# Optimization experiments

Measured on AMD Instinct MI355X. Metric: run time of the kernel, lower is better.

Reference implementation:

```python
import jax, jax.numpy as jnp
import numpy as np

GROUPS = 32
EPS = 1e-3  # keras GroupNormalization default epsilon

def group_norm(x, gamma, beta):
    B, H, W, C = x.shape
    g = GROUPS
    xg = x.reshape(B, H, W, g, C // g)
    mean = jnp.mean(xg, axis=(1, 2, 4), keepdims=True)
    var = jnp.var(xg, axis=(1, 2, 4), keepdims=True)
    xn = (xg - mean) * jax.lax.rsqrt(var + EPS)
    xn = xn.reshape(B, H, W, C)
    return xn * gamma + beta

def setup_inputs() -> dict:
    key = jax.random.key(0)
    ks = jax.random.split(key, 8)
    B, H, W, C = 16, 32, 32, 512
    s = C ** -0.5
    return {
        "x": jax.random.normal(ks[0], (B, H, W, C), jnp.float32),
        "gamma": jnp.ones((C,), jnp.float32),
        "beta": jnp.zeros((C,), jnp.float32),
        "wq": jax.random.normal(ks[1], (C, C), jnp.float32) * s,
        "bq": jnp.zeros((C,), jnp.float32),
        "wk": jax.random.normal(ks[2], (C, C), jnp.float32) * s,
        "bk": jnp.zeros((C,), jnp.float32),
        "wv": jax.random.normal(ks[3], (C, C), jnp.float32) * s,
        "bv": jnp.zeros((C,), jnp.float32),
        "wp": jax.random.normal(ks[4], (C, C), jnp.float32) * s,
        "bp": jnp.zeros((C,), jnp.float32),
        "index": 0,
    }

def reference(x, gamma, beta, wq, bq, wk, bk, wv, bv, wp, bp, index):
    B, H, W, C = x.shape
    N = H * W
    residual = x
    xn = group_norm(x, gamma, beta)
    xf = xn.reshape(B, N, C)
    q = xf @ wq + bq
    k = xf @ wk + bk
    v = xf @ wv + bv
    # full self-attention over all H*W positions (single head)
    scores = jnp.einsum('bnc,bmc->bnm', q, k) * (C ** -0.5)  # [B, N, N]
    attn = jax.nn.softmax(scores, axis=-1)
    out = jnp.einsum('bnm,bmc->bnc', attn, v)
    out = out @ wp + bp
    return out.reshape(B, H, W, C) + residual
```

## Files before the change

kernel.cpp:

```cpp
#include <hip/hip_runtime.h>

typedef __bf16 bf16;
typedef __bf16 bf16x8 __attribute__((ext_vector_type(8)));
typedef __bf16 bf16x4 __attribute__((ext_vector_type(4)));
typedef float  f32x4  __attribute__((ext_vector_type(4)));

#define CDIM   512
#define NPOS   1024
#define NBATCH 16
#define MTOT   (NBATCH * NPOS)
#define WELEMS (CDIM * CDIM)

#define OFF_WT  ((size_t)0)
#define OFF_XN  ((size_t)(2 * 1024 * 1024))
#define OFF_Q   (OFF_XN + (size_t)MTOT * CDIM * 2)
#define OFF_K   (OFF_Q  + (size_t)MTOT * CDIM * 2)
#define OFF_VT  (OFF_K  + (size_t)MTOT * CDIM * 2)
#define OFF_O   OFF_XN

__device__ __forceinline__ void gload16(const bf16* g, bf16* l) {
    __builtin_amdgcn_global_load_lds(
        (const __attribute__((address_space(1))) void*)g,
        (__attribute__((address_space(3))) void*)l, 16, 0, 0);
}

__device__ __forceinline__ unsigned int pk2(float lo, float hi) {
    union { bf16 h; unsigned short s; } a, c;
    a.h = (bf16)lo; c.h = (bf16)hi;
    return (unsigned int)a.s | ((unsigned int)c.s << 16);
}

__global__ __launch_bounds__(256) void transpose_cast(
    const float* __restrict__ w0, const float* __restrict__ w1,
    const float* __restrict__ w2, const float* __restrict__ w3,
    bf16* __restrict__ wt)
{
    __shared__ bf16 tile[32][33];
    int z = blockIdx.z;
    const float* W = (z == 0) ? w0 : (z == 1) ? w1 : (z == 2) ? w2 : w3;
    bf16* out = wt + (size_t)z * WELEMS;
    int bx = blockIdx.x * 32;
    int by = blockIdx.y * 32;
    int tx = threadIdx.x & 31, ty = threadIdx.x >> 5;
    #pragma unroll
    for (int i = ty; i < 32; i += 8)
        tile[i][tx] = (bf16)W[(size_t)(by + i) * CDIM + bx + tx];
    __syncthreads();
    #pragma unroll
    for (int i = ty; i < 32; i += 8)
        out[(size_t)(bx + i) * CDIM + by + tx] = tile[tx][i];
}

__global__ __launch_bounds__(256) void groupnorm_kernel(
    const float* __restrict__ x, const float* __restrict__ gamma,
    const float* __restrict__ beta, bf16* __restrict__ xn)
{
    int b = blockIdx.x >> 5;
    int g = blockIdx.x & 31;
    const float* xb = x + (size_t)b * NPOS * CDIM;
    int t = threadIdx.x, lane = t & 63, wid = t >> 6;

    float s = 0.f, s2 = 0.f;
    for (int i = t; i < 4096; i += 256) {
        int n = i >> 2, c4 = i & 3;
        const float4 v = *(const float4*)&xb[n * CDIM + g * 16 + c4 * 4];
        s  += v.x + v.y + v.z + v.w;
        s2 += v.x * v.x + v.y * v.y + v.z * v.z + v.w * v.w;
    }
    #pragma unroll
    for (int o = 32; o; o >>= 1) { s += __shfl_xor(s, o); s2 += __shfl_xor(s2, o); }
    __shared__ float rs[4], rs2[4];
    if (lane == 0) { rs[wid] = s; rs2[wid] = s2; }
    __syncthreads();
    float S  = rs[0] + rs[1] + rs[2] + rs[3];
    float S2 = rs2[0] + rs2[1] + rs2[2] + rs2[3];
    const float inv_n = 1.f / 16384.f;
    float mean = S * inv_n;
    float var  = S2 * inv_n - mean * mean;
    float rstd = rsqrtf(var + 1e-3f);

    bf16* xnb = xn + (size_t)b * NPOS * CDIM;
    for (int i = t; i < 4096; i += 256) {
        int n = i >> 2, c4 = i & 3;
        int c = g * 16 + c4 * 4;
        const float4 v = *(const float4*)&xb[n * CDIM + c];
        bf16x4 o;
        o[0] = (bf16)(((v.x - mean) * rstd) * gamma[c + 0] + beta[c + 0]);
        o[1] = (bf16)(((v.y - mean) * rstd) * gamma[c + 1] + beta[c + 1]);
        o[2] = (bf16)(((v.z - mean) * rstd) * gamma[c + 2] + beta[c + 2]);
        o[3] = (bf16)(((v.w - mean) * rstd) * gamma[c + 3] + beta[c + 3]);
        *(bf16x4*)&xnb[n * CDIM + c] = o;
    }
}

#define BM 128
#define BN 128
#define BK 32

__global__ __launch_bounds__(256) void gemm_qkv(
    const bf16* __restrict__ A, const bf16* __restrict__ Bw,
    const float* __restrict__ bq, const float* __restrict__ bk,
    const float* __restrict__ bv, float qscale,
    bf16* __restrict__ Qo, bf16* __restrict__ Ko, bf16* __restrict__ Vto)
{
    __shared__ __align__(16) bf16 lsa[BM * BK];
    __shared__ __align__(16) bf16 lsb[BN * BK];
    const int bm = blockIdx.x * BM;
    const int bnG = blockIdx.y * BN;
    const int region = blockIdx.y >> 2;
    const int t = threadIdx.x;
    const int lane = t & 63;
    const int wid = t >> 6;
    const int wr = (wid >> 1) * 64;
    const int wc = (wid & 1) * 64;
    const int lr = lane & 15;
    const int ks = lane >> 4;

    const int r0 = t >> 2, c0 = (t & 3) * 8;
    const int r1 = (t + 256) >> 2, c1 = ((t + 256) & 3) * 8;

    f32x4 acc[4][4] = {};

    for (int k0 = 0; k0 < CDIM; k0 += BK) {
        gload16(&A[(size_t)(bm + r0) * CDIM + k0 + c0], &lsa[t * 8]);
        gload16(&A[(size_t)(bm + r1) * CDIM + k0 + c1], &lsa[(t + 256) * 8]);
        gload16(&Bw[(size_t)(bnG + r0) * CDIM + k0 + c0], &lsb[t * 8]);
        gload16(&Bw[(size_t)(bnG + r1) * CDIM + k0 + c1], &lsb[(t + 256) * 8]);
        __syncthreads();
        bf16x8 af[4], bfr[4];
        #pragma unroll
        for (int m = 0; m < 4; m++)
            af[m] = *(const bf16x8*)&lsa[(wr + m * 16 + lr) * BK + ks * 8];
        #pragma unroll
        for (int n = 0; n < 4; n++)
            bfr[n] = *(const bf16x8*)&lsb[(wc + n * 16 + lr) * BK + ks * 8];
        #pragma unroll
        for (int m = 0; m < 4; m++)
            #pragma unroll
            for (int n = 0; n < 4; n++)
                acc[m][n] = __builtin_amdgcn_mfma_f32_16x16x32_bf16(af[m], bfr[n], acc[m][n], 0, 0, 0);
        __syncthreads();
    }

    const float* bias = (region == 0) ? bq : (region == 1) ? bk : bv;
    const float scale = (region == 0) ? qscale : 1.f;
    #pragma unroll
    for (int m = 0; m < 4; m++) {
        #pragma unroll
        for (int n = 0; n < 4; n++) {
            const int row0 = bm + wr + m * 16 + ks * 4;
            const int colG = bnG + wc + n * 16 + lr;
            const int cl = colG - region * CDIM;
            const float bvl = bias[cl];
            #pragma unroll
            for (int r = 0; r < 4; r++) {
                const int rr = row0 + r;
                const float v = (acc[m][n][r] + bvl) * scale;
                if (region == 0) {
                    Qo[(size_t)rr * CDIM + cl] = (bf16)v;
                } else if (region == 1) {
                    Ko[(size_t)rr * CDIM + cl] = (bf16)v;
                } else {
                    const int bb = rr >> 10, nn = rr & 1023;
                    Vto[(size_t)bb * CDIM * NPOS + (size_t)cl * NPOS + nn] = (bf16)v;
                }
            }
        }
    }
}

#define QT 64
#define KVB 64

__global__ __launch_bounds__(256, 1) void flash_attn(
    const bf16* __restrict__ Q, const bf16* __restrict__ K,
    const bf16* __restrict__ Vt, bf16* __restrict__ O)
{
    __shared__ __align__(16) bf16 Klds[KVB * CDIM];
    __shared__ __align__(16) bf16 Vlds[CDIM * KVB];
    __shared__ unsigned int Plds[4][16 * 35];

    const int p  = blockIdx.x;
    const int b  = (p & 7) + 8 * ((p >> 3) >> 4);
    const int qt = (p >> 3) & 15;

    const int t = threadIdx.x;
    const int lane = t & 63;
    const int w = t >> 6;
    const int lr = lane & 15;
    const int g  = lane >> 4;

    const bf16* Qg = Q  + ((size_t)b * NPOS + qt * QT) * CDIM;
    const bf16* Kg = K  + (size_t)b * NPOS * CDIM;
    const bf16* Vg = Vt + (size_t)b * CDIM * NPOS;

    bf16x8 qf[16];
    {
        const bf16* qrow = Qg + (size_t)(w * 16 + lr) * CDIM + g * 8;
        #pragma unroll
        for (int ds = 0; ds < 16; ds++)
            qf[ds] = *(const bf16x8*)(qrow + ds * 32);
    }

    f32x4 acc[32];
    #pragma unroll
    for (int i = 0; i < 32; i++) acc[i] = (f32x4){0.f, 0.f, 0.f, 0.f};
    float m_run = -1e30f, l_run = 0.f;
    unsigned int* Pw = Plds[w];

    #pragma unroll
    for (int i = 0; i < 16; i++) {
        int ci = t + i * 256;
        int r = ci >> 6, c = ci & 63;
        gload16(Kg + (size_t)r * CDIM + ((c ^ (r & 7)) * 8), &Klds[ci * 8]);
    }
    __syncthreads();

    for (int kt = 0; kt < 16; kt++) {
        {
            const int kv0 = kt * KVB;
            #pragma unroll
            for (int i = 0; i < 16; i++) {
                int ci = t + i * 256;
                int r = ci >> 3, c = ci & 7;
                gload16(Vg + (size_t)r * NPOS + kv0 + ((c ^ (r & 7)) * 8), &Vlds[ci * 8]);
            }
        }
        f32x4 s[4] = {};
        #pragma unroll
        for (int ds = 0; ds < 16; ds++) {
            #pragma unroll
            for (int k16 = 0; k16 < 4; k16++) {
                const int row = k16 * 16 + lr;
                const bf16x8 kf = *(const bf16x8*)&Klds[row * CDIM + (((ds * 4 + g) ^ (row & 7)) * 8)];
                s[k16] = __builtin_amdgcn_mfma_f32_16x16x32_bf16(kf, qf[ds], s[k16], 0, 0, 0);
            }
        }
        float mt = -1e30f;
        #pragma unroll
        for (int k16 = 0; k16 < 4; k16++)
            #pragma unroll
            for (int r = 0; r < 4; r++) mt = fmaxf(mt, s[k16][r]);
        mt = fmaxf(mt, __shfl_xor(mt, 16));
        mt = fmaxf(mt, __shfl_xor(mt, 32));
        const float m_new = (mt > m_run + 8.f) ? mt : m_run;
        float pr[16];
        float ts = 0.f;
        #pragma unroll
        for (int k16 = 0; k16 < 4; k16++)
            #pragma unroll
            for (int r = 0; r < 4; r++) {
                float e = __expf(s[k16][r] - m_new);
                pr[k16 * 4 + r] = e; ts += e;
            }
        ts += __shfl_xor(ts, 16);
        ts += __shfl_xor(ts, 32);
        if (__any(m_new != m_run)) {
            const float alpha = __expf(m_run - m_new);
            #pragma unroll
            for (int i = 0; i < 32; i++) {
                acc[i][0] *= alpha; acc[i][1] *= alpha;
                acc[i][2] *= alpha; acc[i][3] *= alpha;
            }
            l_run *= alpha;
        }
        l_run += ts;
        m_run = m_new;
        #pragma unroll
        for (int k16 = 0; k16 < 4; k16++) {
            Pw[lr * 35 + 8 * k16 + 2 * g + 0] = pk2(pr[k16 * 4 + 0], pr[k16 * 4 + 1]);
            Pw[lr * 35 + 8 * k16 + 2 * g + 1] = pk2(pr[k16 * 4 + 2], pr[k16 * 4 + 3]);
        }
        __syncthreads();
        if (kt < 15) {
            const int kv0 = (kt + 1) * KVB;
            #pragma unroll
            for (int i = 0; i < 16; i++) {
                int ci = t + i * 256;
                int r = ci >> 6, c = ci & 63;
                gload16(Kg + (size_t)(kv0 + r) * CDIM + ((c ^ (r & 7)) * 8), &Klds[ci * 8]);
            }
        }
        bf16x8 pf[2];
        #pragma unroll
        for (int ks2 = 0; ks2 < 2; ks2++) {
            union { unsigned int u[4]; bf16x8 v; } cvt;
            #pragma unroll
            for (int j = 0; j < 4; j++)
                cvt.u[j] = Pw[lr * 35 + ks2 * 16 + g * 4 + j];
            pf[ks2] = cvt.v;
        }
        #pragma unroll
        for (int d16 = 0; d16 < 32; d16++) {
            const int row = d16 * 16 + lr;
            #pragma unroll
            for (int ks2 = 0; ks2 < 2; ks2++) {
                const bf16x8 vf = *(const bf16x8*)&Vlds[row * KVB + (((ks2 * 4 + g) ^ (row & 7)) * 8)];
                acc[d16] = __builtin_amdgcn_mfma_f32_16x16x32_bf16(vf, pf[ks2], acc[d16], 0, 0, 0);
            }
        }
        __syncthreads();
    }

    const float inv = 1.f / l_run;
    bf16* Og = O + ((size_t)b * NPOS + qt * QT + w * 16 + lr) * CDIM;
    #pragma unroll
    for (int d16 = 0; d16 < 32; d16++) {
        bf16x4 o;
        o[0] = (bf16)(acc[d16][0] * inv); o[1] = (bf16)(acc[d16][1] * inv);
        o[2] = (bf16)(acc[d16][2] * inv); o[3] = (bf16)(acc[d16][3] * inv);
        *(bf16x4*)(Og + d16 * 16 + g * 4) = o;
    }
}

__global__ __launch_bounds__(256) void gemm_proj(
    const bf16* __restrict__ A, const bf16* __restrict__ Bw,
    const float* __restrict__ bias, float* __restrict__ Cp,
    const float* __restrict__ resid)
{
    __shared__ __align__(16) bf16 lsa[BM * BK];
    __shared__ __align__(16) bf16 lsb[BN * BK];
    const int bm = blockIdx.x * BM;
    const int bn = blockIdx.y * BN;
    const int t = threadIdx.x;
    const int lane = t & 63;
    const int wid = t >> 6;
    const int wr = (wid >> 1) * 64;
    const int wc = (wid & 1) * 64;
    const int lr = lane & 15;
    const int ks = lane >> 4;
    const int r0 = t >> 2, c0 = (t & 3) * 8;
    const int r1 = (t + 256) >> 2, c1 = ((t + 256) & 3) * 8;

    f32x4 acc[4][4] = {};
    for (int k0 = 0; k0 < CDIM; k0 += BK) {
        gload16(&A[(size_t)(bm + r0) * CDIM + k0 + c0], &lsa[t * 8]);
        gload16(&A[(size_t)(bm + r1) * CDIM + k0 + c1], &lsa[(t + 256) * 8]);
        gload16(&Bw[(size_t)(bn + r0) * CDIM + k0 + c0], &lsb[t * 8]);
        gload16(&Bw[(size_t)(bn + r1) * CDIM + k0 + c1], &lsb[(t + 256) * 8]);
        __syncthreads();
        bf16x8 af[4], bfr[4];
        #pragma unroll
        for (int m = 0; m < 4; m++)
            af[m] = *(const bf16x8*)&lsa[(wr + m * 16 + lr) * BK + ks * 8];
        #pragma unroll
        for (int n = 0; n < 4; n++)
            bfr[n] = *(const bf16x8*)&lsb[(wc + n * 16 + lr) * BK + ks * 8];
        #pragma unroll
        for (int m = 0; m < 4; m++)
            #pragma unroll
            for (int n = 0; n < 4; n++)
                acc[m][n] = __builtin_amdgcn_mfma_f32_16x16x32_bf16(af[m], bfr[n], acc[m][n], 0, 0, 0);
        __syncthreads();
    }
    #pragma unroll
    for (int m = 0; m < 4; m++) {
        #pragma unroll
        for (int n = 0; n < 4; n++) {
            const int row0 = bm + wr + m * 16 + ks * 4;
            const int col  = bn + wc + n * 16 + lr;
            const float bvl = bias[col];
            #pragma unroll
            for (int r = 0; r < 4; r++) {
                const size_t idx = (size_t)(row0 + r) * CDIM + col;
                Cp[idx] = acc[m][n][r] + bvl + resid[idx];
            }
        }
    }
}

extern "C" void kernel_launch(void* const* d_in, const int* in_sizes, int n_in,
                              void* d_out, int out_size, void* d_ws, size_t ws_size,
                              hipStream_t stream) {
    const float* x     = (const float*)d_in[0];
    const float* gamma = (const float*)d_in[1];
    const float* beta  = (const float*)d_in[2];
    const float* wq    = (const float*)d_in[3];
    const float* bq    = (const float*)d_in[4];
    const float* wk    = (const float*)d_in[5];
    const float* bk    = (const float*)d_in[6];
    const float* wv    = (const float*)d_in[7];
    const float* bv    = (const float*)d_in[8];
    const float* wp    = (const float*)d_in[9];
    const float* bp    = (const float*)d_in[10];

    char* ws = (char*)d_ws;
    bf16* wt = (bf16*)(ws + OFF_WT);
    bf16* xn = (bf16*)(ws + OFF_XN);
    bf16* Q  = (bf16*)(ws + OFF_Q);
    bf16* Km = (bf16*)(ws + OFF_K);
    bf16* Vt = (bf16*)(ws + OFF_VT);
    bf16* O  = (bf16*)(ws + OFF_O);

    transpose_cast<<<dim3(16, 16, 4), 256, 0, stream>>>(wq, wk, wv, wp, wt);
    groupnorm_kernel<<<dim3(512), 256, 0, stream>>>(x, gamma, beta, xn);

    const float qscale = 0.04419417382415922f;
    gemm_qkv<<<dim3(128, 12), 256, 0, stream>>>(
        xn, wt, bq, bk, bv, qscale, Q, Km, Vt);

    flash_attn<<<dim3(256), 256, 0, stream>>>(Q, Km, Vt, O);

    gemm_proj<<<dim3(128, 4), 256, 0, stream>>>(
        O, wt + (size_t)3 * WELEMS, bp, (float*)d_out, x);
}
```

Baseline: 261.3 us.

## Split attention across 8 waves, double-buffer K, XCD-aware GEMM tile mapping

```diff
diff --git a/kernel.cpp b/kernel.cpp
--- a/kernel.cpp
+++ b/kernel.cpp
@@ -105,9 +105,14 @@
 {
     __shared__ __align__(16) bf16 lsa[BM * BK];
     __shared__ __align__(16) bf16 lsb[BN * BK];
-    const int bm = blockIdx.x * BM;
-    const int bnG = blockIdx.y * BN;
-    const int region = blockIdx.y >> 2;
+    const int bid = blockIdx.x;
+    const int xcd = bid & 7;
+    const int local = bid >> 3;
+    const int colT = local % 12;
+    const int rowT = (xcd << 4) + local / 12;
+    const int bm = rowT * BM;
+    const int bnG = colT * BN;
+    const int region = colT >> 2;
     const int t = threadIdx.x;
     const int lane = t & 63;
     const int wid = t >> 6;
@@ -170,15 +175,15 @@
 }
 
 #define QT 64
-#define KVB 64
-
-__global__ __launch_bounds__(256, 1) void flash_attn(
+#define KVB 32
+
+__global__ __launch_bounds__(512, 2) void flash_attn(
     const bf16* __restrict__ Q, const bf16* __restrict__ K,
     const bf16* __restrict__ Vt, bf16* __restrict__ O)
 {
-    __shared__ __align__(16) bf16 Klds[KVB * CDIM];
-    __shared__ __align__(16) bf16 Vlds[CDIM * KVB];
-    __shared__ unsigned int Plds[4][16 * 35];
+    __shared__ __align__(16) bf16 Klds[2][KVB * CDIM];
+    __shared__ unsigned int Pw[4][16 * 20];
+    __shared__ float Mx[4][2][16], Tx[4][2][16];
 
     const int p  = blockIdx.x;
     const int b  = (p & 7) + 8 * ((p >> 3) >> 4);
@@ -187,125 +192,117 @@
     const int t = threadIdx.x;
     const int lane = t & 63;
     const int w = t >> 6;
+    const int wq = w & 3;
+    const int wd = w >> 2;
     const int lr = lane & 15;
     const int g  = lane >> 4;
 
     const bf16* Qg = Q  + ((size_t)b * NPOS + qt * QT) * CDIM;
     const bf16* Kg = K  + (size_t)b * NPOS * CDIM;
-    const bf16* Vg = Vt + (size_t)b * CDIM * NPOS;
+    const bf16* Vg = Vt + (size_t)b * CDIM * NPOS + (size_t)(wd * 256) * NPOS;
 
     bf16x8 qf[16];
     {
-        const bf16* qrow = Qg + (size_t)(w * 16 + lr) * CDIM + g * 8;
-        #pragma unroll
-        for (int ds = 0; ds < 16; ds++)
-            qf[ds] = *(const bf16x8*)(qrow + ds * 32);
-    }
-
-    f32x4 acc[32];
-    #pragma unroll
-    for (int i = 0; i < 32; i++) acc[i] = (f32x4){0.f, 0.f, 0.f, 0.f};
+        const bf16* qrow = Qg + (size_t)(wq * 16 + lr) * CDIM + g * 8;
+        #pragma unroll
+        for (int ds = 0; ds < 16; ds++) qf[ds] = *(const bf16x8*)(qrow + ds * 32);
+    }
+
+    f32x4 acc[16] = {};
     float m_run = -1e30f, l_run = 0.f;
-    unsigned int* Pw = Plds[w];
-
-    #pragma unroll
-    for (int i = 0; i < 16; i++) {
-        int ci = t + i * 256;
+
+    #pragma unroll
+    for (int i = 0; i < 4; i++) {
+        int ci = t + i * 512;
         int r = ci >> 6, c = ci & 63;
-        gload16(Kg + (size_t)r * CDIM + ((c ^ (r & 7)) * 8), &Klds[ci * 8]);
+        gload16(Kg + (size_t)r * CDIM + ((c ^ (r & 7)) * 8), &Klds[0][ci * 8]);
     }
     __syncthreads();
 
-    for (int kt = 0; kt < 16; kt++) {
-        {
-            const int kv0 = kt * KVB;
-            #pragma unroll
-            for (int i = 0; i < 16; i++) {
-                int ci = t + i * 256;
-                int r = ci >> 3, c = ci & 7;
-                gload16(Vg + (size_t)r * NPOS + kv0 + ((c ^ (r & 7)) * 8), &Vlds[ci * 8]);
+    for (int kt = 0; kt < 32; kt++) {
+        const int cur = kt & 1;
+        const int kv0 = kt * KVB;
+
+        bf16x8 vf[16];
+        #pragma unroll
+        for (int d16 = 0; d16 < 16; d16++)
+            vf[d16] = *(const bf16x8*)&Vg[(size_t)(d16 * 16 + lr) * NPOS + kv0 + g * 8];
+
+        if (kt < 31) {
+            const bf16* Kn = Kg + (size_t)(kv0 + KVB) * CDIM;
+            #pragma unroll
+            for (int i = 0; i < 4; i++) {
+                int ci = t + i * 512;
+                int r = ci >> 6, c = ci & 63;
+                gload16(Kn + (size_t)r * CDIM + ((c ^ (r & 7)) * 8), &Klds[cur ^ 1][ci * 8]);
             }
         }
-        f32x4 s[4] = {};
-        #pragma unroll
-        for (int ds = 0; ds < 16; ds++) {
-            #pragma unroll
-            for (int k16 = 0; k16 < 4; k16++) {
-                const int row = k16 * 16 + lr;
-                const bf16x8 kf = *(const bf16x8*)&Klds[row * CDIM + (((ds * 4 + g) ^ (row & 7)) * 8)];
-                s[k16] = __builtin_amdgcn_mfma_f32_16x16x32_bf16(kf, qf[ds], s[k16], 0, 0, 0);
-            }
-        }
-        float mt = -1e30f;
-        #pragma unroll
-        for (int k16 = 0; k16 < 4; k16++)
-            #pragma unroll
-            for (int r = 0; r < 4; r++) mt = fmaxf(mt, s[k16][r]);
+
+        const int krow = wd * 16 + lr;
+        const bf16* kb = &Klds[cur][krow * CDIM];
+        f32x4 sa = {}, sb = {}, sc = {}, sd = {};
+        #pragma unroll
+        for (int ds = 0; ds < 4; ds++) {
+            const bf16x8 k0 = *(const bf16x8*)&kb[(((ds +  0) * 4 + g) ^ (lr & 7)) * 8];
+            const bf16x8 k1 = *(const bf16x8*)&kb[(((ds +  4) * 4 + g) ^ (lr & 7)) * 8];
+            const bf16x8 k2 = *(const bf16x8*)&kb[(((ds +  8) * 4 + g) ^ (lr & 7)) * 8];
+            const bf16x8 k3 = *(const bf16x8*)&kb[(((ds + 12) * 4 + g) ^ (lr & 7)) * 8];
+            sa = __builtin_amdgcn_mfma_f32_16x16x32_bf16(k0, qf[ds +  0], sa, 0, 0, 0);
+            sb = __builtin_amdgcn_mfma_f32_16x16x32_bf16(k1, qf[ds +  4], sb, 0, 0, 0);
+            sc = __builtin_amdgcn_mfma_f32_16x16x32_bf16(k2, qf[ds +  8], sc, 0, 0, 0);
+            sd = __builtin_amdgcn_mfma_f32_16x16x32_bf16(k3, qf[ds + 12], sd, 0, 0, 0);
+        }
+        f32x4 s;
+        #pragma unroll
+        for (int i = 0; i < 4; i++) s[i] = (sa[i] + sb[i]) + (sc[i] + sd[i]);
+
+        float mt = fmaxf(fmaxf(s[0], s[1]), fmaxf(s[2], s[3]));
         mt = fmaxf(mt, __shfl_xor(mt, 16));
         mt = fmaxf(mt, __shfl_xor(mt, 32));
-        const float m_new = (mt > m_run + 8.f) ? mt : m_run;
-        float pr[16];
-        float ts = 0.f;
-        #pragma unroll
-        for (int k16 = 0; k16 < 4; k16++)
-            #pragma unroll
-            for (int r = 0; r < 4; r++) {
-                float e = __expf(s[k16][r] - m_new);
-                pr[k16 * 4 + r] = e; ts += e;
-            }
+        if (lane < 16) Mx[wq][wd][lane] = mt;
+        __syncthreads();
+
+        const float mfull = fmaxf(mt, Mx[wq][wd ^ 1][lr]);
+        const float m_new = (mfull > m_run + 8.f) ? mfull : m_run;
+        const float p0 = __expf(s[0] - m_new), p1 = __expf(s[1] - m_new);
+        const float p2 = __expf(s[2] - m_new), p3 = __expf(s[3] - m_new);
+        float ts = p0 + p1 + p2 + p3;
         ts += __shfl_xor(ts, 16);
         ts += __shfl_xor(ts, 32);
+        if (lane < 16) Tx[wq][wd][lane] = ts;
+        Pw[wq][lr * 20 + wd * 8 + g * 2 + 0] = pk2(p0, p1);
+        Pw[wq][lr * 20 + wd * 8 + g * 2 + 1] = pk2(p2, p3);
+        __syncthreads();
+
+        const float tsf = ts + Tx[wq][wd ^ 1][lr];
         if (__any(m_new != m_run)) {
             const float alpha = __expf(m_run - m_new);
             #pragma unroll
-            for (int i = 0; i < 32; i++) {
+            for (int i = 0; i < 16; i++) {
                 acc[i][0] *= alpha; acc[i][1] *= alpha;
                 acc[i][2] *= alpha; acc[i][3] *= alpha;
             }
             l_run *= alpha;
         }
-        l_run += ts;
+        l_run += tsf;
         m_run = m_new;
-        #pragma unroll
-        for (int k16 = 0; k16 < 4; k16++) {
-            Pw[lr * 35 + 8 * k16 + 2 * g + 0] = pk2(pr[k16 * 4 + 0], pr[k16 * 4 + 1]);
-            Pw[lr * 35 + 8 * k16 + 2 * g + 1] = pk2(pr[k16 * 4 + 2], pr[k16 * 4 + 3]);
-        }
-        __syncthreads();
-        if (kt < 15) {
-            const int kv0 = (kt + 1) * KVB;
-            #pragma unroll
-            for (int i = 0; i < 16; i++) {
-                int ci = t + i * 256;
-                int r = ci >> 6, c = ci & 63;
-                gload16(Kg + (size_t)(kv0 + r) * CDIM + ((c ^ (r & 7)) * 8), &Klds[ci * 8]);
-            }
-        }
-        bf16x8 pf[2];
-        #pragma unroll
-        for (int ks2 = 0; ks2 < 2; ks2++) {
-            union { unsigned int u[4]; bf16x8 v; } cvt;
-            #pragma unroll
-            for (int j = 0; j < 4; j++)
-                cvt.u[j] = Pw[lr * 35 + ks2 * 16 + g * 4 + j];
-            pf[ks2] = cvt.v;
-        }
-        #pragma unroll
-        for (int d16 = 0; d16 < 32; d16++) {
-            const int row = d16 * 16 + lr;
-            #pragma unroll
-            for (int ks2 = 0; ks2 < 2; ks2++) {
-                const bf16x8 vf = *(const bf16x8*)&Vlds[row * KVB + (((ks2 * 4 + g) ^ (row & 7)) * 8)];
-                acc[d16] = __builtin_amdgcn_mfma_f32_16x16x32_bf16(vf, pf[ks2], acc[d16], 0, 0, 0);
-            }
-        }
-        __syncthreads();
+
+        bf16x8 pf;
+        {
+            union { unsigned int u[4]; bf16x8 v; } cv;
+            #pragma unroll
+            for (int j = 0; j < 4; j++) cv.u[j] = Pw[wq][lr * 20 + g * 4 + j];
+            pf = cv.v;
+        }
+        #pragma unroll
+        for (int d16 = 0; d16 < 16; d16++)
+            acc[d16] = __builtin_amdgcn_mfma_f32_16x16x32_bf16(vf[d16], pf, acc[d16], 0, 0, 0);
     }
 
     const float inv = 1.f / l_run;
-    bf16* Og = O + ((size_t)b * NPOS + qt * QT + w * 16 + lr) * CDIM;
-    #pragma unroll
-    for (int d16 = 0; d16 < 32; d16++) {
+    bf16* Og = O + ((size_t)b * NPOS + qt * QT + wq * 16 + lr) * CDIM + wd * 256;
+    #pragma unroll
+    for (int d16 = 0; d16 < 16; d16++) {
         bf16x4 o;
         o[0] = (bf16)(acc[d16][0] * inv); o[1] = (bf16)(acc[d16][1] * inv);
         o[2] = (bf16)(acc[d16][2] * inv); o[3] = (bf16)(acc[d16][3] * inv);
@@ -320,8 +317,13 @@
 {
     __shared__ __align__(16) bf16 lsa[BM * BK];
     __shared__ __align__(16) bf16 lsb[BN * BK];
-    const int bm = blockIdx.x * BM;
-    const int bn = blockIdx.y * BN;
+    const int bid = blockIdx.x;
+    const int xcd = bid & 7;
+    const int local = bid >> 3;
+    const int colT = local & 3;
+    const int rowT = (xcd << 4) + (local >> 2);
+    const int bm = rowT * BM;
+    const int bn = colT * BN;
     const int t = threadIdx.x;
     const int lane = t & 63;
     const int wid = t >> 6;
@@ -396,11 +398,11 @@
     groupnorm_kernel<<<dim3(512), 256, 0, stream>>>(x, gamma, beta, xn);
 
     const float qscale = 0.04419417382415922f;
-    gemm_qkv<<<dim3(128, 12), 256, 0, stream>>>(
+    gemm_qkv<<<dim3(1536), 256, 0, stream>>>(
         xn, wt, bq, bk, bv, qscale, Q, Km, Vt);
 
-    flash_attn<<<dim3(256), 256, 0, stream>>>(Q, Km, Vt, O);
-
-    gemm_proj<<<dim3(128, 4), 256, 0, stream>>>(
+    flash_attn<<<dim3(256), 512, 0, stream>>>(Q, Km, Vt, O);
+
+    gemm_proj<<<dim3(512), 256, 0, stream>>>(
         O, wt + (size_t)3 * WELEMS, bp, (float*)d_out, x);
 }
```

New measurement: 367.4 us. +40.6%, slower.
